# Kernel optimization log

Measured on AMD Instinct MI355X. Metric: run time of the kernel, lower is better.

Reference implementation:

```python
import jax, jax.numpy as jnp
import numpy as np

RNN_DIMS = 1024
FC_DIMS = 1024
N_CLASSES = 256
BATCH = 128


def setup_inputs() -> dict:
    key = jax.random.key(0)
    ks = jax.random.split(key, 10)
    s = 1.0 / np.sqrt(RNN_DIMS)
    inp = {
        "x": jax.random.normal(ks[0], (BATCH, RNN_DIMS), dtype=jnp.float32),
        "h1": jax.random.normal(ks[1], (BATCH, RNN_DIMS), dtype=jnp.float32),
        # GRUCell params (PyTorch layout: [3*H, H] stacked as r,z,n)
        "w_ih": jax.random.uniform(ks[2], (3 * RNN_DIMS, RNN_DIMS), jnp.float32, -s, s),
        "w_hh": jax.random.uniform(ks[3], (3 * RNN_DIMS, RNN_DIMS), jnp.float32, -s, s),
        "b_ih": jax.random.uniform(ks[4], (3 * RNN_DIMS,), jnp.float32, -s, s),
        "b_hh": jax.random.uniform(ks[5], (3 * RNN_DIMS,), jnp.float32, -s, s),
        "w_fc1": jax.random.uniform(ks[6], (FC_DIMS, RNN_DIMS), jnp.float32, -s, s),
        "b_fc1": jax.random.uniform(ks[7], (FC_DIMS,), jnp.float32, -s, s),
        "w_fc3": jax.random.uniform(ks[8], (N_CLASSES, FC_DIMS), jnp.float32, -1.0 / np.sqrt(FC_DIMS), 1.0 / np.sqrt(FC_DIMS)),
        "b_fc3": jax.random.uniform(ks[9], (N_CLASSES,), jnp.float32, -1.0 / np.sqrt(FC_DIMS), 1.0 / np.sqrt(FC_DIMS)),
    }
    return inp


def reference(x, h1, w_ih, w_hh, b_ih, b_hh, w_fc1, b_fc1, w_fc3, b_fc3):
    # --- GRUCell (PyTorch semantics) ---
    gi = x @ w_ih.T + b_ih          # [B, 3H]
    gh = h1 @ w_hh.T + b_hh         # [B, 3H]
    i_r, i_z, i_n = jnp.split(gi, 3, axis=-1)
    h_r, h_z, h_n = jnp.split(gh, 3, axis=-1)
    r = jax.nn.sigmoid(i_r + h_r)
    z = jax.nn.sigmoid(i_z + h_z)
    n = jnp.tanh(i_n + r * h_n)
    h1_prime = (1.0 - z) * n + z * h1   # [B, H]
    # --- residual + MLP head ---
    res = h1_prime + x
    relu1 = jax.nn.relu(res @ w_fc1.T + b_fc1)   # [B, FC]
    out = relu1 @ w_fc3.T + b_fc3                # [B, N_CLASSES]
    return (out, h1_prime)
```

## Files before the change

kernel.cpp:

```cpp
#include <hip/hip_runtime.h>
#include <math.h>

typedef short bf16x8 __attribute__((ext_vector_type(8)));
typedef float f32x4 __attribute__((ext_vector_type(4)));

__device__ __forceinline__ int cvt2(float lo, float hi) {
    int r;
    asm("v_cvt_pk_bf16_f32 %0, %1, %2" : "=v"(r) : "v"(lo), "v"(hi));
    return r;
}

template<int NT, bool ATOMIC, bool RELUA>
__global__ __launch_bounds__(256, 2) void gemm_k(
    const float* __restrict__ act0, const float* __restrict__ wgt0,
    const float* __restrict__ act1, const float* __restrict__ wgt1,
    int split, const float* __restrict__ bias,
    float* __restrict__ out, int ldo, int nkt, int ksbits)
{
    constexpr int CT = NT / 16;
    __shared__ short As[2][64 * 64];
    __shared__ short Ws[2][NT * 64];

    const int tid  = threadIdx.x;
    const int lane = tid & 63;
    const int wv   = tid >> 6;

    const int ks   = blockIdx.x & ((1 << ksbits) - 1);
    const int rest = blockIdx.x >> ksbits;
    const int rg   = rest & 1;
    const int tile = rest >> 1;
    const int c0   = tile * NT;
    const int row0 = rg * 64;
    const int kt0  = ks * nkt;

    const float* act = act0;
    const float* wgt = wgt0;
    int wr0 = c0;
    if (c0 >= split) { act = act1; wgt = wgt1; wr0 = c0 - split; }

    const int r0 = tid >> 3, kc = tid & 7;
    const float* aP = act + (row0 + r0) * 1024 + kt0 * 64 + kc * 8;
    const float* wP = wgt + (wr0 + r0) * 1024 + kt0 * 64 + kc * 8;
    const bool wAct = (tid < NT * 8);

    const int saI0 = (r0 * 64 + kc * 8) ^ ((r0 & 7) << 3);
    const int saI1 = ((r0 + 32) * 64 + kc * 8) ^ ((r0 & 7) << 3);

    f32x4 A[4][4], W[4][2];
    f32x4 acc[CT] = {};

#define ISSUE(kt, s) do {                                                 \
        A[s][0] = *(const f32x4*)(aP + (kt) * 64);                        \
        A[s][1] = *(const f32x4*)(aP + (kt) * 64 + 4);                    \
        A[s][2] = *(const f32x4*)(aP + (kt) * 64 + 32768);                \
        A[s][3] = *(const f32x4*)(aP + (kt) * 64 + 32772);                \
        if (wAct) {                                                       \
            W[s][0] = *(const f32x4*)(wP + (kt) * 64);                    \
            W[s][1] = *(const f32x4*)(wP + (kt) * 64 + 4);                \
        }                                                                 \
    } while (0)

#define RL(x) (RELUA ? fmaxf((x), 0.0f) : (x))

#define STAGE(s, b) do {                                                  \
        int4 p0, p1;                                                      \
        p0.x = cvt2(RL(A[s][0][0]), RL(A[s][0][1]));                      \
        p0.y = cvt2(RL(A[s][0][2]), RL(A[s][0][3]));                      \
        p0.z = cvt2(RL(A[s][1][0]), RL(A[s][1][1]));                      \
        p0.w = cvt2(RL(A[s][1][2]), RL(A[s][1][3]));                      \
        p1.x = cvt2(RL(A[s][2][0]), RL(A[s][2][1]));                      \
        p1.y = cvt2(RL(A[s][2][2]), RL(A[s][2][3]));                      \
        p1.z = cvt2(RL(A[s][3][0]), RL(A[s][3][1]));                      \
        p1.w = cvt2(RL(A[s][3][2]), RL(A[s][3][3]));                      \
        *(int4*)&As[b][saI0] = p0;                                        \
        *(int4*)&As[b][saI1] = p1;                                        \
        if (wAct) {                                                       \
            int4 q;                                                       \
            q.x = cvt2(W[s][0][0], W[s][0][1]);                           \
            q.y = cvt2(W[s][0][2], W[s][0][3]);                           \
            q.z = cvt2(W[s][1][0], W[s][1][1]);                           \
            q.w = cvt2(W[s][1][2], W[s][1][3]);                           \
            *(int4*)&Ws[b][saI0] = q;                                     \
        }                                                                 \
    } while (0)

#define COMPUTE(b) do {                                                   \
        _Pragma("unroll")                                                 \
        for (int kk = 0; kk < 64; kk += 32) {                             \
            const int kw = kk + 8 * (lane >> 4);                          \
            const int ar = wv * 16 + (lane & 15);                         \
            bf16x8 af = *(const bf16x8*)&As[b][(ar * 64 + kw) ^ ((ar & 7) << 3)]; \
            bf16x8 bw[CT];                                                \
            _Pragma("unroll")                                             \
            for (int ct = 0; ct < CT; ++ct) {                             \
                int br = ct * 16 + (lane & 15);                           \
                bw[ct] = *(const bf16x8*)&Ws[b][(br * 64 + kw) ^ ((br & 7) << 3)]; \
            }                                                             \
            _Pragma("unroll")                                             \
            for (int ct = 0; ct < CT; ++ct)                               \
                acc[ct] = __builtin_amdgcn_mfma_f32_16x16x32_bf16(        \
                    af, bw[ct], acc[ct], 0, 0, 0);                        \
        }                                                                 \
    } while (0)

#define BAR() do {                                                        \
        asm volatile("s_waitcnt lgkmcnt(0)" ::: "memory");                \
        __builtin_amdgcn_s_barrier();                                     \
        __builtin_amdgcn_sched_barrier(0);                                \
    } while (0)

    ISSUE(0, 0); ISSUE(1, 1); ISSUE(2, 2); ISSUE(3, 3);

    #pragma unroll 1
    for (int g = 0; g < nkt / 4; ++g) {
        const int kt = 4 * g;
        STAGE(0, 0); if (kt + 4 < nkt) ISSUE(kt + 4, 0); BAR(); COMPUTE(0);
        STAGE(1, 1); if (kt + 5 < nkt) ISSUE(kt + 5, 1); BAR(); COMPUTE(1);
        STAGE(2, 0); if (kt + 6 < nkt) ISSUE(kt + 6, 2); BAR(); COMPUTE(0);
        STAGE(3, 1); if (kt + 7 < nkt) ISSUE(kt + 7, 3); BAR(); COMPUTE(1);
    }

#undef ISSUE
#undef RL
#undef STAGE
#undef COMPUTE
#undef BAR

    #pragma unroll
    for (int ct = 0; ct < CT; ++ct) {
        int col = c0 + ct * 16 + (lane & 15);
        float bv = (bias && ks == 0) ? bias[col] : 0.0f;
        #pragma unroll
        for (int r = 0; r < 4; ++r) {
            int row = row0 + wv * 16 + (lane >> 4) * 4 + r;
            float v = acc[ct][r] + bv;
            if (ATOMIC) unsafeAtomicAdd(&out[row * ldo + col], v);
            else        out[row * ldo + col] = v;
        }
    }
}

__global__ __launch_bounds__(256) void gru_k(
    const float* __restrict__ g, const float* __restrict__ x,
    const float* __restrict__ h1,
    const float* __restrict__ b_ih, const float* __restrict__ b_hh,
    float* __restrict__ h1p_out, float* __restrict__ res,
    float* __restrict__ zero_f1p, float* __restrict__ zero_out)
{
    int id = blockIdx.x * 256 + threadIdx.x;
    zero_f1p[id] = 0.0f;
    if (id < 128 * 256) zero_out[id] = 0.0f;
    int m = id >> 10, j = id & 1023;
    const float* gr = g + m * 6144;
    float ir  = gr[j]        + b_ih[j];
    float iz  = gr[1024 + j] + b_ih[1024 + j];
    float in_ = gr[2048 + j] + b_ih[2048 + j];
    float hr  = gr[3072 + j] + b_hh[j];
    float hz  = gr[4096 + j] + b_hh[1024 + j];
    float hn  = gr[5120 + j] + b_hh[2048 + j];
    float r = 1.0f / (1.0f + __expf(-(ir + hr)));
    float z = 1.0f / (1.0f + __expf(-(iz + hz)));
    float n = tanhf(in_ + r * hn);
    float hp = (1.0f - z) * n + z * h1[id];
    h1p_out[id] = hp;
    res[id] = hp + x[id];
}

extern "C" void kernel_launch(void* const* d_in, const int* in_sizes, int n_in,
                              void* d_out, int out_size, void* d_ws, size_t ws_size,
                              hipStream_t stream)
{
    const float* x     = (const float*)d_in[0];
    const float* h1    = (const float*)d_in[1];
    const float* w_ih  = (const float*)d_in[2];
    const float* w_hh  = (const float*)d_in[3];
    const float* b_ih  = (const float*)d_in[4];
    const float* b_hh  = (const float*)d_in[5];
    const float* w_fc1 = (const float*)d_in[6];
    const float* b_fc1 = (const float*)d_in[7];
    const float* w_fc3 = (const float*)d_in[8];
    const float* b_fc3 = (const float*)d_in[9];

    float* out = (float*)d_out;
    float* h1p = out + 128 * 256;

    float* ws  = (float*)d_ws;
    float* g   = ws;
    float* res = ws + 128 * 6144;
    float* f1p = res + 128 * 1024;

    gemm_k<32, false, false><<<384, 256, 0, stream>>>(
        x, w_ih, h1, w_hh, 3072, nullptr, g, 6144, 16, 0);
    gru_k<<<512, 256, 0, stream>>>(g, x, h1, b_ih, b_hh, h1p, res, f1p, out);
    gemm_k<16, true, false><<<256, 256, 0, stream>>>(
        res, w_fc1, res, w_fc1, 1 << 30, b_fc1, f1p, 1024, 8, 1);
    gemm_k<16, true, true><<<64, 256, 0, stream>>>(
        f1p, w_fc3, f1p, w_fc3, 1 << 30, b_fc3, out, 256, 8, 1);
}
```

Baseline: 31.75 us.

## Fuse GRU gate GEMMs with pointwise GRU cell into one kernel

Replaces the gate GEMM plus separate GRU elementwise kernel with a single kernel. Each block computes all six gate slices (r,z,n for both input and hidden) for a 16-column tile and 64 rows, then applies the GRU cell in registers. This removes the 128x6144 gate intermediate round-trip through global memory and one launch. The cost is fewer blocks (128 vs 384), a larger per-block LDS footprint and more register pressure, which could reduce parallelism.

Result: faster. 30.20 us (-4.9%).

```diff
diff --git a/kernel.cpp b/kernel.cpp
--- a/kernel.cpp
+++ b/kernel.cpp
@@ -10,11 +10,150 @@
     return r;
 }
 
+#define BAR() do {                                                        \
+        asm volatile("s_waitcnt lgkmcnt(0)" ::: "memory");                \
+        __builtin_amdgcn_s_barrier();                                     \
+        __builtin_amdgcn_sched_barrier(0);                                \
+    } while (0)
+
+__global__ __launch_bounds__(256, 2) void gates_k(
+    const float* __restrict__ x, const float* __restrict__ h1,
+    const float* __restrict__ w_ih, const float* __restrict__ w_hh,
+    const float* __restrict__ b_ih, const float* __restrict__ b_hh,
+    float* __restrict__ h1p, float* __restrict__ res,
+    float* __restrict__ zf1p, float* __restrict__ zout)
+{
+    __shared__ short As[2][128 * 64];
+    __shared__ short Ws[2][96 * 64];
+    const int tid  = threadIdx.x;
+    const int lane = tid & 63;
+    const int wv   = tid >> 6;
+
+    {
+        int id = blockIdx.x * 256 + tid;
+        f32x4 z = {};
+        *(f32x4*)(zf1p + id * 4) = z;
+        zout[id] = 0.0f;
+    }
+
+    const int b    = blockIdx.x;
+    const int tile = (b & 7) * 8 + ((b >> 3) >> 1);
+    const int rg   = (b >> 3) & 1;
+    const int c0   = tile * 16;
+    const int row0 = rg * 64;
+
+    const int r0 = tid >> 3, kc = tid & 7;
+
+    const float* aP[4];
+    int saI[4];
+    #pragma unroll
+    for (int i = 0; i < 4; ++i) {
+        int ma = r0 + 32 * i;
+        const float* src = (i < 2) ? x : h1;
+        aP[i] = src + (row0 + (ma & 63)) * 1024 + kc * 8;
+        saI[i] = (ma * 64 + kc * 8) ^ ((ma & 7) << 3);
+    }
+    const float* wP[3];
+    int swI[3];
+    #pragma unroll
+    for (int i = 0; i < 3; ++i) {
+        int mw = r0 + 32 * i;
+        int g = mw >> 4;
+        const float* src = (g < 3) ? w_ih : w_hh;
+        wP[i] = src + ((g % 3) * 1024 + c0 + (mw & 15)) * 1024 + kc * 8;
+        swI[i] = (mw * 64 + kc * 8) ^ ((mw & 7) << 3);
+    }
+
+    f32x4 A[2][4][2], W[2][3][2];
+    f32x4 acc[6] = {};
+
+#define G_ISSUE(kt, s) do {                                               \
+        _Pragma("unroll")                                                 \
+        for (int i = 0; i < 4; ++i) {                                     \
+            A[s][i][0] = *(const f32x4*)(aP[i] + (kt) * 64);              \
+            A[s][i][1] = *(const f32x4*)(aP[i] + (kt) * 64 + 4);          \
+        }                                                                 \
+        _Pragma("unroll")                                                 \
+        for (int i = 0; i < 3; ++i) {                                     \
+            W[s][i][0] = *(const f32x4*)(wP[i] + (kt) * 64);              \
+            W[s][i][1] = *(const f32x4*)(wP[i] + (kt) * 64 + 4);          \
+        }                                                                 \
+    } while (0)
+
+#define G_STAGE(s, bb) do {                                               \
+        _Pragma("unroll")                                                 \
+        for (int i = 0; i < 4; ++i) {                                     \
+            int4 p;                                                       \
+            p.x = cvt2(A[s][i][0][0], A[s][i][0][1]);                     \
+            p.y = cvt2(A[s][i][0][2], A[s][i][0][3]);                     \
+            p.z = cvt2(A[s][i][1][0], A[s][i][1][1]);                     \
+            p.w = cvt2(A[s][i][1][2], A[s][i][1][3]);                     \
+            *(int4*)&As[bb][saI[i]] = p;                                  \
+        }                                                                 \
+        _Pragma("unroll")                                                 \
+        for (int i = 0; i < 3; ++i) {                                     \
+            int4 q;                                                       \
+            q.x = cvt2(W[s][i][0][0], W[s][i][0][1]);                     \
+            q.y = cvt2(W[s][i][0][2], W[s][i][0][3]);                     \
+            q.z = cvt2(W[s][i][1][0], W[s][i][1][1]);                     \
+            q.w = cvt2(W[s][i][1][2], W[s][i][1][3]);                     \
+            *(int4*)&Ws[bb][swI[i]] = q;                                  \
+        }                                                                 \
+    } while (0)
+
+#define G_COMPUTE(bb) do {                                                \
+        _Pragma("unroll")                                                 \
+        for (int kk = 0; kk < 64; kk += 32) {                             \
+            const int kw = kk + 8 * (lane >> 4);                          \
+            const int ar = wv * 16 + (lane & 15);                         \
+            bf16x8 afx = *(const bf16x8*)&As[bb][(ar * 64 + kw) ^ ((ar & 7) << 3)]; \
+            bf16x8 afh = *(const bf16x8*)&As[bb][((ar + 64) * 64 + kw) ^ ((ar & 7) << 3)]; \
+            _Pragma("unroll")                                             \
+            for (int g = 0; g < 6; ++g) {                                 \
+                int br = g * 16 + (lane & 15);                            \
+                bf16x8 bw = *(const bf16x8*)&Ws[bb][(br * 64 + kw) ^ ((br & 7) << 3)]; \
+                acc[g] = __builtin_amdgcn_mfma_f32_16x16x32_bf16(         \
+                    (g < 3) ? afx : afh, bw, acc[g], 0, 0, 0);            \
+            }                                                             \
+        }                                                                 \
+    } while (0)
+
+    G_ISSUE(0, 0); G_ISSUE(1, 1);
+
+    #pragma unroll 1
+    for (int kt2 = 0; kt2 < 8; ++kt2) {
+        const int kt = 2 * kt2;
+        G_STAGE(0, 0); if (kt + 2 < 16) G_ISSUE(kt + 2, 0); BAR(); G_COMPUTE(0);
+        G_STAGE(1, 1); if (kt + 3 < 16) G_ISSUE(kt + 3, 1); BAR(); G_COMPUTE(1);
+    }
+
+#undef G_ISSUE
+#undef G_STAGE
+#undef G_COMPUTE
+
+    const int j = c0 + (lane & 15);
+    const float bir = b_ih[j], biz = b_ih[1024 + j], bin = b_ih[2048 + j];
+    const float bhr = b_hh[j], bhz = b_hh[1024 + j], bhn = b_hh[2048 + j];
+    const int rbase = row0 + wv * 16 + (lane >> 4) * 4;
+    #pragma unroll
+    for (int r = 0; r < 4; ++r) {
+        const int row = rbase + r;
+        float ir  = acc[0][r] + bir, iz = acc[1][r] + biz, inn = acc[2][r] + bin;
+        float hr  = acc[3][r] + bhr, hz = acc[4][r] + bhz, hn  = acc[5][r] + bhn;
+        float rr = 1.0f / (1.0f + __expf(-(ir + hr)));
+        float zz = 1.0f / (1.0f + __expf(-(iz + hz)));
+        float nn = tanhf(inn + rr * hn);
+        float h1v = h1[row * 1024 + j];
+        float hp  = (1.0f - zz) * nn + zz * h1v;
+        h1p[row * 1024 + j] = hp;
+        res[row * 1024 + j] = hp + x[row * 1024 + j];
+    }
+}
+
 template<int NT, bool ATOMIC, bool RELUA>
 __global__ __launch_bounds__(256, 2) void gemm_k(
-    const float* __restrict__ act0, const float* __restrict__ wgt0,
-    const float* __restrict__ act1, const float* __restrict__ wgt1,
-    int split, const float* __restrict__ bias,
+    const float* __restrict__ act, const float* __restrict__ wgt,
+    const float* __restrict__ bias,
     float* __restrict__ out, int ldo, int nkt, int ksbits)
 {
     constexpr int CT = NT / 16;
@@ -33,14 +172,9 @@
     const int row0 = rg * 64;
     const int kt0  = ks * nkt;
 
-    const float* act = act0;
-    const float* wgt = wgt0;
-    int wr0 = c0;
-    if (c0 >= split) { act = act1; wgt = wgt1; wr0 = c0 - split; }
-
     const int r0 = tid >> 3, kc = tid & 7;
     const float* aP = act + (row0 + r0) * 1024 + kt0 * 64 + kc * 8;
-    const float* wP = wgt + (wr0 + r0) * 1024 + kt0 * 64 + kc * 8;
+    const float* wP = wgt + (c0 + r0) * 1024 + kt0 * 64 + kc * 8;
     const bool wAct = (tid < NT * 8);
 
     const int saI0 = (r0 * 64 + kc * 8) ^ ((r0 & 7) << 3);
@@ -60,7 +194,7 @@
         }                                                                 \
     } while (0)
 
-#define RL(x) (RELUA ? fmaxf((x), 0.0f) : (x))
+#define RL(v) (RELUA ? fmaxf((v), 0.0f) : (v))
 
 #define STAGE(s, b) do {                                                  \
         int4 p0, p1;                                                      \
@@ -103,12 +237,6 @@
         }                                                                 \
     } while (0)
 
-#define BAR() do {                                                        \
-        asm volatile("s_waitcnt lgkmcnt(0)" ::: "memory");                \
-        __builtin_amdgcn_s_barrier();                                     \
-        __builtin_amdgcn_sched_barrier(0);                                \
-    } while (0)
-
     ISSUE(0, 0); ISSUE(1, 1); ISSUE(2, 2); ISSUE(3, 3);
 
     #pragma unroll 1
@@ -124,7 +252,6 @@
 #undef RL
 #undef STAGE
 #undef COMPUTE
-#undef BAR
 
     #pragma unroll
     for (int ct = 0; ct < CT; ++ct) {
@@ -138,32 +265,6 @@
             else        out[row * ldo + col] = v;
         }
     }
-}
-
-__global__ __launch_bounds__(256) void gru_k(
-    const float* __restrict__ g, const float* __restrict__ x,
-    const float* __restrict__ h1,
-    const float* __restrict__ b_ih, const float* __restrict__ b_hh,
-    float* __restrict__ h1p_out, float* __restrict__ res,
-    float* __restrict__ zero_f1p, float* __restrict__ zero_out)
-{
-    int id = blockIdx.x * 256 + threadIdx.x;
-    zero_f1p[id] = 0.0f;
-    if (id < 128 * 256) zero_out[id] = 0.0f;
-    int m = id >> 10, j = id & 1023;
-    const float* gr = g + m * 6144;
-    float ir  = gr[j]        + b_ih[j];
-    float iz  = gr[1024 + j] + b_ih[1024 + j];
-    float in_ = gr[2048 + j] + b_ih[2048 + j];
-    float hr  = gr[3072 + j] + b_hh[j];
-    float hz  = gr[4096 + j] + b_hh[1024 + j];
-    float hn  = gr[5120 + j] + b_hh[2048 + j];
-    float r = 1.0f / (1.0f + __expf(-(ir + hr)));
-    float z = 1.0f / (1.0f + __expf(-(iz + hz)));
-    float n = tanhf(in_ + r * hn);
-    float hp = (1.0f - z) * n + z * h1[id];
-    h1p_out[id] = hp;
-    res[id] = hp + x[id];
 }
 
 extern "C" void kernel_launch(void* const* d_in, const int* in_sizes, int n_in,
@@ -185,15 +286,13 @@
     float* h1p = out + 128 * 256;
 
     float* ws  = (float*)d_ws;
-    float* g   = ws;
-    float* res = ws + 128 * 6144;
-    float* f1p = res + 128 * 1024;
-
-    gemm_k<32, false, false><<<384, 256, 0, stream>>>(
-        x, w_ih, h1, w_hh, 3072, nullptr, g, 6144, 16, 0);
-    gru_k<<<512, 256, 0, stream>>>(g, x, h1, b_ih, b_hh, h1p, res, f1p, out);
+    float* res = ws;
+    float* f1p = ws + 128 * 1024;
+
+    gates_k<<<128, 256, 0, stream>>>(x, h1, w_ih, w_hh, b_ih, b_hh,
+                                     h1p, res, f1p, out);
     gemm_k<16, true, false><<<256, 256, 0, stream>>>(
-        res, w_fc1, res, w_fc1, 1 << 30, b_fc1, f1p, 1024, 8, 1);
+        res, w_fc1, b_fc1, f1p, 1024, 8, 1);
     gemm_k<16, true, true><<<64, 256, 0, stream>>>(
-        f1p, w_fc3, f1p, w_fc3, 1 << 30, b_fc3, out, 256, 8, 1);
-}
+        f1p, w_fc3, b_fc3, out, 256, 8, 1);
+}
```
